# Optimization experiments

Measured on AMD Instinct MI355X. Metric: run time of the kernel, lower is better.

The kernel has to match this reference:

```python
import jax, jax.numpy as jnp
import numpy as np

NUM_USERS = 60000
NUM_ITEMS = 40000
N_NODES = NUM_USERS + NUM_ITEMS
EMBED_K = 128
E_HALF = 1_000_000  # bipartite interactions; symmetrized -> 2M directed edges


def setup_inputs() -> dict:
    key = jax.random.key(0)
    k1, k2, k3, k4, k5, k6, k7 = jax.random.split(key, 7)
    scale = 1.0 / np.sqrt(EMBED_K)  # ~ xavier_normal
    Gu = jax.random.normal(k1, (NUM_USERS, EMBED_K), jnp.float32) * scale
    Gi = jax.random.normal(k2, (NUM_ITEMS, EMBED_K), jnp.float32) * scale
    W0 = jax.random.normal(k3, (EMBED_K, EMBED_K), jnp.float32) * scale
    W1 = jax.random.normal(k4, (EMBED_K, EMBED_K), jnp.float32) * scale
    W2 = jax.random.normal(k5, (EMBED_K, EMBED_K), jnp.float32) * scale
    # bipartite user-item graph, symmetrized (items offset by NUM_USERS)
    u = jax.random.randint(k6, (E_HALF,), 0, NUM_USERS)
    it = jax.random.randint(k7, (E_HALF,), 0, NUM_ITEMS) + NUM_USERS
    src = jnp.concatenate([u, it])
    dst = jnp.concatenate([it, u])
    edge_index = jnp.stack([src, dst]).astype(jnp.int32)  # [2, 2M]
    return {"Gu": Gu, "Gi": Gi, "W0": W0, "W1": W1, "W2": W2,
            "edge_index": edge_index}


def reference(Gu, Gi, W0, W1, W2, edge_index):
    # add_self_loops=False, bias=False) -> ReLU), then split into (gu, gi).
    src, dst = edge_index[0], edge_index[1]
    n_users = Gu.shape[0]
    n_nodes = Gu.shape[0] + Gi.shape[0]
    # PyG gcn_norm (no self loops): deg = scatter(1, col); norm = d^-1/2[row]*d^-1/2[col]
    ones = jnp.ones(src.shape, Gu.dtype)
    deg = jax.ops.segment_sum(ones, dst, num_segments=n_nodes)
    dinv = jnp.where(deg > 0, jax.lax.rsqrt(jnp.maximum(deg, 1.0)), 0.0)
    norm = dinv[src] * dinv[dst]  # [E]
    x = jnp.concatenate([Gu, Gi], axis=0)  # [N, d]
    for W in (W0, W1, W2):
        h = x @ W                                   # [N, d] dense GEMM
        msg = h[src] * norm[:, None]                # [E, d] gather + scale
        x = jax.nn.relu(jax.ops.segment_sum(msg, dst, num_segments=n_nodes))
    return x[:n_users], x[n_users:]
```

## Files before the change

### kernel.cpp

```cpp
#include <hip/hip_runtime.h>
#include <hip/hip_bf16.h>

#define EMB 128
#define NPB 256
#define NB_PAD 512
#define CHUNK 4096
#define FILL_CAP 7168
#define CU_CAP 4864
#define CI_CAP 7168

typedef unsigned int uint32;
typedef unsigned long long uint64;
typedef __attribute__((ext_vector_type(8))) short bf16x8;
typedef __attribute__((ext_vector_type(4))) float f32x4;
typedef __attribute__((ext_vector_type(2))) float f32x2;
typedef __attribute__((ext_vector_type(2))) unsigned int uint32x2;

__device__ __forceinline__ ushort f2bf(float f) {
    uint32 u = __float_as_uint(f);
    return (ushort)((u + 0x7fff + ((u >> 16) & 1)) >> 16);
}
__device__ __forceinline__ uint32 pack_hi2(uint32 u0, uint32 u1) {
    return (u1 & 0xffff0000u) | (u0 >> 16);
}
__device__ __forceinline__ float blo(uint32 u) { return __uint_as_float(u << 16); }
__device__ __forceinline__ float bhi(uint32 u) { return __uint_as_float(u & 0xffff0000u); }

__device__ __forceinline__ int region_base(int b, int UB) {
    return (b < UB) ? b * CU_CAP : UB * CU_CAP + (b - UB) * CI_CAP;
}


__global__ __launch_bounds__(256) void wsplit_kernel(
    const float* __restrict__ W0, const float* __restrict__ W1,
    const float* __restrict__ W2,
    ushort* __restrict__ Whi, ushort* __restrict__ Wlo,
    int* __restrict__ gcursor, int NB, int UB) {
    int wsel = blockIdx.x >> 4, part = blockIdx.x & 15;
    if (blockIdx.x == 0) {
        for (int b = threadIdx.x; b < NB; b += 256) gcursor[b] = region_base(b, UB);
    }
    const float* W = (wsel == 0) ? W0 : (wsel == 1) ? W1 : W2;
    ushort* hiT = Whi + wsel * EMB * EMB;
    ushort* loT = Wlo + wsel * EMB * EMB;
    int i0 = part * 1024;
    #pragma unroll
    for (int j = 0; j < 4; j++) {
        int i = i0 + threadIdx.x + j * 256;
        int k = i >> 7, n = i & 127;
        float w = W[i];
        uint32 u = __float_as_uint(w);
        ushort hi = (ushort)(u >> 16);
        float hif = __uint_as_float(u & 0xffff0000u);
        ushort lo = f2bf(w - hif);
        hiT[n * EMB + k] = hi;
        loT[n * EMB + k] = lo;
    }
}


__global__ __launch_bounds__(256) void bucket_scatter_kernel(
    const int* __restrict__ src, const int* __restrict__ dst,
    int* __restrict__ gcursor, uint2* __restrict__ ebuf, int E, int NB) {
    __shared__ int cnt[NB_PAD];
    __shared__ int loff[NB_PAD];
    __shared__ int gbase[NB_PAD];
    __shared__ int pos[NB_PAD];
    __shared__ int sc[256];
    __shared__ uint2 stage[CHUNK];
    int t = threadIdx.x;
    long e0 = (long)blockIdx.x * CHUNK;
    int n = E - (int)e0; if (n > CHUNK) n = CHUNK;
    for (int b = t; b < NB_PAD; b += 256) { cnt[b] = 0; pos[b] = 0; }
    __syncthreads();
    int es[CHUNK / 256], ed[CHUNK / 256];
    #pragma unroll
    for (int i = 0; i < CHUNK / 256; i++) {
        int idx = t + i * 256;
        if (idx < n) {
            es[i] = src[e0 + idx];
            ed[i] = dst[e0 + idx];
            atomicAdd(&cnt[ed[i] >> 8], 1);
        }
    }
    __syncthreads();
    int a = cnt[2 * t], b2 = cnt[2 * t + 1];
    sc[t] = a + b2;
    __syncthreads();
    for (int off = 1; off < 256; off <<= 1) {
        int v = (t >= off) ? sc[t - off] : 0;
        __syncthreads();
        sc[t] += v;
        __syncthreads();
    }
    int excl = sc[t] - (a + b2);
    loff[2 * t] = excl;
    loff[2 * t + 1] = excl + a;
    __syncthreads();
    for (int b = t; b < NB; b += 256)
        if (cnt[b] > 0) gbase[b] = atomicAdd(&gcursor[b], cnt[b]);
    __syncthreads();
    #pragma unroll
    for (int i = 0; i < CHUNK / 256; i++) {
        int idx = t + i * 256;
        if (idx < n) {
            int b = ed[i] >> 8;
            int p = atomicAdd(&pos[b], 1);
            stage[loff[b] + p] = make_uint2((uint32)es[i], (uint32)ed[i]);
        }
    }
    __syncthreads();
    for (int i = t; i < n; i += 256) {
        uint2 e = stage[i];
        int b = (int)e.y >> 8;
        ebuf[gbase[b] + (i - loff[b])] = e;
    }
}


__global__ __launch_bounds__(256) void bucket_deg_kernel(
    const uint2* __restrict__ ebuf, const int* __restrict__ gcursor,
    uint2* __restrict__ nodeRange, float* __restrict__ dinv, int N, int UB) {
    __shared__ int cnt[NPB];
    __shared__ int sc[256];
    int t = threadIdx.x;
    int b = blockIdx.x;
    int n0 = b * NPB;
    int nn = N - n0; if (nn > NPB) nn = NPB;
    cnt[t] = 0;
    __syncthreads();
    int rb = region_base(b, UB);
    int re = gcursor[b];
    for (int e = rb + t; e < re; e += 256) {
        uint2 sd = ebuf[e];
        atomicAdd(&cnt[(int)sd.y - n0], 1);
    }
    __syncthreads();
    int c = cnt[t];
    sc[t] = c;
    __syncthreads();
    for (int off = 1; off < 256; off <<= 1) {
        int v = (t >= off) ? sc[t - off] : 0;
        __syncthreads();
        sc[t] += v;
        __syncthreads();
    }
    int excl = sc[t] - c;
    if (t < nn) {
        int s = rb + excl;
        nodeRange[n0 + t] = make_uint2((uint32)s, (uint32)(s + c));
        dinv[n0 + t] = c > 0 ? rsqrtf((float)c) : 0.0f;
    }
}


__global__ __launch_bounds__(256) void fill_ew_kernel(
    uint2* __restrict__ ebuf, const uint2* __restrict__ nodeRange,
    const int* __restrict__ gcursor, const float* __restrict__ dinv,
    int N, int UB) {
    __shared__ uint2 stage[FILL_CAP];
    __shared__ int cnt[NPB];
    __shared__ int rp[NPB];
    int t = threadIdx.x;
    int b = blockIdx.x;
    int n0 = b * NPB;
    int nn = N - n0; if (nn > NPB) nn = NPB;
    if (t < nn) { cnt[t] = 0; rp[t] = (int)nodeRange[n0 + t].x; }
    __syncthreads();
    int e0 = region_base(b, UB);
    int e1 = gcursor[b];
    int ecount = e1 - e0; if (ecount > FILL_CAP) ecount = FILL_CAP;
    for (int o = t; o < ecount; o += 256) stage[o] = ebuf[e0 + o];
    __syncthreads();
    for (int o = t; o < ecount; o += 1024) {
        uint2 sd[4]; int pos[4]; float wv[4];
        int valid = 0;
        #pragma unroll
        for (int k = 0; k < 4; k++) {
            int oo = o + k * 256;
            if (oo < ecount) { sd[k] = stage[oo]; valid = k + 1; }
        }
        #pragma unroll
        for (int k = 0; k < 4; k++)
            if (k < valid) {
                int local = (int)sd[k].y - n0;
                pos[k] = rp[local] + atomicAdd(&cnt[local], 1);
            }
        #pragma unroll
        for (int k = 0; k < 4; k++)
            if (k < valid) wv[k] = dinv[(int)sd[k].x];
        #pragma unroll
        for (int k = 0; k < 4; k++)
            if (k < valid) ebuf[pos[k]] = make_uint2(sd[k].x, __float_as_uint(wv[k]));
    }
}


template<int DI>
__device__ __forceinline__ void agg_tail2(
    const uint32x2* __restrict__ Yh2, const uint2* __restrict__ ew,
    int base, int e0, int e1, int half, int l32,
    float& a0, float& a1, float& a2, float& a3) {
    uint32 rows[DI]; float w[DI]; uint32x2 p[DI];
    #pragma unroll
    for (int k = 0; k < DI; k++) {
        int i0 = base + 2 * k, i1 = i0 + 1;
        uint2 s0 = ew[i0 < e1 ? i0 : e0];
        uint2 s1 = ew[i1 < e1 ? i1 : e0];
        rows[k] = half ? s1.x : s0.x;
        uint32 wu = half ? s1.y : s0.y;
        w[k] = (i0 + half < e1) ? __uint_as_float(wu) : 0.0f;
    }
    #pragma unroll
    for (int k = 0; k < DI; k++) p[k] = Yh2[(size_t)rows[k] * 32 + l32];
    #pragma unroll
    for (int k = 0; k < DI; k++) {
        a0 += w[k] * blo(p[k].x); a1 += w[k] * bhi(p[k].x);
        a2 += w[k] * blo(p[k].y); a3 += w[k] * bhi(p[k].y);
    }
}

__device__ __forceinline__ void agg_node2(
    const uint32x2* __restrict__ Yh2, const uint2* __restrict__ ew,
    int e0, int e1, int half, int l32,
    float& a0, float& a1, float& a2, float& a3) {
    int base = e0;
    for (; base + 16 <= e1; base += 16) {
        uint32 rows[8]; float w[8]; uint32x2 p[8];
        #pragma unroll
        for (int k = 0; k < 8; k++) {
            uint2 s0 = ew[base + 2 * k];
            uint2 s1 = ew[base + 2 * k + 1];
            rows[k] = half ? s1.x : s0.x;
            w[k] = __uint_as_float(half ? s1.y : s0.y);
        }
        #pragma unroll
        for (int k = 0; k < 8; k++) p[k] = Yh2[(size_t)rows[k] * 32 + l32];
        #pragma unroll
        for (int k = 0; k < 8; k++) {
            a0 += w[k] * blo(p[k].x); a1 += w[k] * bhi(p[k].x);
            a2 += w[k] * blo(p[k].y); a3 += w[k] * bhi(p[k].y);
        }
    }
    int rem = e1 - base;
    if (rem > 8)      agg_tail2<8>(Yh2, ew, base, e0, e1, half, l32, a0, a1, a2, a3);
    else if (rem > 4) agg_tail2<4>(Yh2, ew, base, e0, e1, half, l32, a0, a1, a2, a3);
    else if (rem > 2) agg_tail2<2>(Yh2, ew, base, e0, e1, half, l32, a0, a1, a2, a3);
    else if (rem > 0) agg_tail2<1>(Yh2, ew, base, e0, e1, half, l32, a0, a1, a2, a3);
}

__global__ __launch_bounds__(256) void agg_relu_kernel(
    const uint32x2* __restrict__ Yh2,
    const uint2* __restrict__ nodeRange, const uint2* __restrict__ ew,
    const float* __restrict__ dinv, float* __restrict__ out, int N) {
    int node = blockIdx.x * 4 + (threadIdx.x >> 6);
    if (node >= N) return;
    int lane = threadIdx.x & 63;
    int half = lane >> 5, l32 = lane & 31;
    uint2 rg = nodeRange[node];
    int e0 = __builtin_amdgcn_readfirstlane((int)rg.x);
    int e1 = __builtin_amdgcn_readfirstlane((int)rg.y);
    float a0 = 0.f, a1 = 0.f, a2 = 0.f, a3 = 0.f;
    agg_node2(Yh2, ew, e0, e1, half, l32, a0, a1, a2, a3);
    a0 += __shfl_xor(a0, 32);
    a1 += __shfl_xor(a1, 32);
    a2 += __shfl_xor(a2, 32);
    a3 += __shfl_xor(a3, 32);
    if (half == 0) {
        float wd = dinv[node];
        f32x4 r = { fmaxf(a0 * wd, 0.f), fmaxf(a1 * wd, 0.f),
                    fmaxf(a2 * wd, 0.f), fmaxf(a3 * wd, 0.f) };
        __builtin_nontemporal_store(r, (f32x4*)(out + (size_t)node * EMB + l32 * 4));
    }
}


union FragU { uint32 u[4]; bf16x8 v; };

__global__ __launch_bounds__(256, 2) void gemm_mfma_kernel(
    const float* __restrict__ A, const float* __restrict__ A2, int Msplit,
    const ushort* __restrict__ WhiT, const ushort* __restrict__ WloT,
    ushort* __restrict__ Yh, int M) {
    __shared__ float As[16][132];
    int t = threadIdx.x;
    int wv = t >> 6, lane = t & 63, quad = lane >> 4, l16 = lane & 15;

    FragU bfr[8][2];
    #pragma unroll
    for (int kc = 0; kc < 8; kc++) {
        const ushort* srcW = (kc < 4) ? WhiT : WloT;
        int kb = (kc & 3) * 32 + quad * 8;
        #pragma unroll
        for (int c = 0; c < 2; c++) {
            int n = wv * 32 + c * 16 + l16;
            const uint32* p = (const uint32*)(srcW + n * EMB + kb);
            bfr[kc][c].u[0] = p[0];
            bfr[kc][c].u[1] = p[1];
            bfr[kc][c].u[2] = p[2];
            bfr[kc][c].u[3] = p[3];
        }
    }

    int srow = t >> 4, skq = t & 15;
    int ntile = (M + 15) >> 4;
    for (int tile = blockIdx.x; tile < ntile; tile += (int)gridDim.x) {
        int r0 = tile << 4;
        __syncthreads();
        {
            float4 v0 = {0.f, 0.f, 0.f, 0.f}, v1 = v0;
            int row = r0 + srow;
            if (row < M) {
                const float* ga = (row < Msplit)
                    ? A  + (size_t)row * EMB + skq * 8
                    : A2 + (size_t)(row - Msplit) * EMB + skq * 8;
                v0 = *(const float4*)ga;
                v1 = *(const float4*)(ga + 4);
            }
            *(float4*)&As[srow][skq * 8] = v0;
            *(float4*)&As[srow][skq * 8 + 4] = v1;
        }
        __syncthreads();

        FragU ah[4], al[4];
        #pragma unroll
        for (int kc = 0; kc < 4; kc++) {
            const float* p = &As[l16][kc * 32 + quad * 8];
            float4 xa = *(const float4*)p;
            float4 xb = *(const float4*)(p + 4);
            uint32 u0 = __float_as_uint(xa.x), u1 = __float_as_uint(xa.y);
            uint32 u2 = __float_as_uint(xa.z), u3 = __float_as_uint(xa.w);
            uint32 u4 = __float_as_uint(xb.x), u5 = __float_as_uint(xb.y);
            uint32 u6 = __float_as_uint(xb.z), u7 = __float_as_uint(xb.w);
            ah[kc].u[0] = pack_hi2(u0, u1);
            ah[kc].u[1] = pack_hi2(u2, u3);
            ah[kc].u[2] = pack_hi2(u4, u5);
            ah[kc].u[3] = pack_hi2(u6, u7);
            float l0 = xa.x - __uint_as_float(u0 & 0xffff0000u);
            float l1 = xa.y - __uint_as_float(u1 & 0xffff0000u);
            float l2 = xa.z - __uint_as_float(u2 & 0xffff0000u);
            float l3 = xa.w - __uint_as_float(u3 & 0xffff0000u);
            float l4 = xb.x - __uint_as_float(u4 & 0xffff0000u);
            float l5 = xb.y - __uint_as_float(u5 & 0xffff0000u);
            float l6 = xb.z - __uint_as_float(u6 & 0xffff0000u);
            float l7 = xb.w - __uint_as_float(u7 & 0xffff0000u);
            al[kc].u[0] = pack_hi2(__float_as_uint(l0), __float_as_uint(l1));
            al[kc].u[1] = pack_hi2(__float_as_uint(l2), __float_as_uint(l3));
            al[kc].u[2] = pack_hi2(__float_as_uint(l4), __float_as_uint(l5));
            al[kc].u[3] = pack_hi2(__float_as_uint(l6), __float_as_uint(l7));
        }

        f32x4 acc0 = {0.f, 0.f, 0.f, 0.f};
        f32x4 acc1 = {0.f, 0.f, 0.f, 0.f};
        #pragma unroll
        for (int kc = 0; kc < 4; kc++) {
            acc0 = __builtin_amdgcn_mfma_f32_16x16x32_bf16(ah[kc].v, bfr[kc][0].v, acc0, 0, 0, 0);
            acc1 = __builtin_amdgcn_mfma_f32_16x16x32_bf16(ah[kc].v, bfr[kc][1].v, acc1, 0, 0, 0);
        }
        #pragma unroll
        for (int kc = 0; kc < 4; kc++) {
            acc0 = __builtin_amdgcn_mfma_f32_16x16x32_bf16(ah[kc].v, bfr[kc + 4][0].v, acc0, 0, 0, 0);
            acc1 = __builtin_amdgcn_mfma_f32_16x16x32_bf16(ah[kc].v, bfr[kc + 4][1].v, acc1, 0, 0, 0);
        }
        #pragma unroll
        for (int kc = 0; kc < 4; kc++) {
            acc0 = __builtin_amdgcn_mfma_f32_16x16x32_bf16(al[kc].v, bfr[kc][0].v, acc0, 0, 0, 0);
            acc1 = __builtin_amdgcn_mfma_f32_16x16x32_bf16(al[kc].v, bfr[kc][1].v, acc1, 0, 0, 0);
        }

        int colb = wv * 32 + l16;
        #pragma unroll
        for (int r = 0; r < 4; r++) {
            int row = r0 + quad * 4 + r;
            if (row < M) {
                Yh[(size_t)row * EMB + colb]      = f2bf(acc0[r]);
                Yh[(size_t)row * EMB + colb + 16] = f2bf(acc1[r]);
            }
        }
    }
}


extern "C" void kernel_launch(void* const* d_in, const int* in_sizes, int n_in,
                              void* d_out, int out_size, void* d_ws, size_t ws_size,
                              hipStream_t stream) {
    (void)n_in; (void)out_size; (void)ws_size;
    const float* Gu = (const float*)d_in[0];
    const float* Gi = (const float*)d_in[1];
    const float* W0 = (const float*)d_in[2];
    const float* W1 = (const float*)d_in[3];
    const float* W2 = (const float*)d_in[4];
    const int* ei = (const int*)d_in[5];

    int nu = in_sizes[0] / EMB;
    int ni = in_sizes[1] / EMB;
    int N = nu + ni;
    int E = in_sizes[5] / 2;
    const int* src = ei;
    const int* dst = ei + E;
    int NB = (N + NPB - 1) / NPB;
    int UB = nu >> 8;
    long ebufEntries = (long)UB * CU_CAP + (long)(NB - UB) * CI_CAP;

    ushort* Yh      = (ushort*)d_ws;
    uint2* ebuf     = (uint2*)(Yh + (size_t)N * EMB);
    uint2* nodeRange= ebuf + ebufEntries;
    float* dinv     = (float*)(nodeRange + N);
    int* gcursor    = (int*)(dinv + N);
    ushort* WhiT    = (ushort*)(gcursor + NB);
    ushort* WloT    = WhiT + 3 * EMB * EMB;
    float* X        = (float*)d_out;

    wsplit_kernel<<<48, 256, 0, stream>>>(W0, W1, W2, WhiT, WloT, gcursor, NB, UB);

    int ecb = (E + CHUNK - 1) / CHUNK;
    bucket_scatter_kernel<<<ecb, 256, 0, stream>>>(src, dst, gcursor, ebuf, E, NB);
    bucket_deg_kernel<<<NB, 256, 0, stream>>>(ebuf, gcursor, nodeRange, dinv, N, UB);
    fill_ew_kernel<<<NB, 256, 0, stream>>>(ebuf, nodeRange, gcursor, dinv, N, UB);

    const uint2* ew = (const uint2*)ebuf;
    int aggBlocks = (N + 3) / 4;
    const int GB = 512;

    gemm_mfma_kernel<<<GB, 256, 0, stream>>>(Gu, Gi, nu, WhiT, WloT, Yh, N);
    agg_relu_kernel<<<aggBlocks, 256, 0, stream>>>((const uint32x2*)Yh, nodeRange, ew, dinv, X, N);
    gemm_mfma_kernel<<<GB, 256, 0, stream>>>(X, X, N, WhiT + EMB * EMB, WloT + EMB * EMB, Yh, N);
    agg_relu_kernel<<<aggBlocks, 256, 0, stream>>>((const uint32x2*)Yh, nodeRange, ew, dinv, X, N);
    gemm_mfma_kernel<<<GB, 256, 0, stream>>>(X, X, N, WhiT + 2 * EMB * EMB, WloT + 2 * EMB * EMB, Yh, N);
    agg_relu_kernel<<<aggBlocks, 256, 0, stream>>>((const uint32x2*)Yh, nodeRange, ew, dinv, X, N);
}
```

Baseline: 414.4 us.

## Fold source normalization into GEMM and compact edges to 32-bit indices

```diff
diff --git a/kernel.cpp b/kernel.cpp
--- a/kernel.cpp
+++ b/kernel.cpp
@@ -10,10 +10,8 @@
 #define CI_CAP 7168
 
 typedef unsigned int uint32;
-typedef unsigned long long uint64;
 typedef __attribute__((ext_vector_type(8))) short bf16x8;
 typedef __attribute__((ext_vector_type(4))) float f32x4;
-typedef __attribute__((ext_vector_type(2))) float f32x2;
 typedef __attribute__((ext_vector_type(2))) unsigned int uint32x2;
 
 __device__ __forceinline__ ushort f2bf(float f) {
@@ -35,10 +33,11 @@
     const float* __restrict__ W0, const float* __restrict__ W1,
     const float* __restrict__ W2,
     ushort* __restrict__ Whi, ushort* __restrict__ Wlo,
-    int* __restrict__ gcursor, int NB, int UB) {
+    int* __restrict__ gcursor, uint32* __restrict__ YhZrow, int NB, int UB) {
     int wsel = blockIdx.x >> 4, part = blockIdx.x & 15;
     if (blockIdx.x == 0) {
         for (int b = threadIdx.x; b < NB; b += 256) gcursor[b] = region_base(b, UB);
+        if (threadIdx.x < 64) YhZrow[threadIdx.x] = 0;
     }
     const float* W = (wsel == 0) ? W0 : (wsel == 1) ? W1 : W2;
     ushort* hiT = Whi + wsel * EMB * EMB;
@@ -61,7 +60,7 @@
 
 __global__ __launch_bounds__(256) void bucket_scatter_kernel(
     const int* __restrict__ src, const int* __restrict__ dst,
-    int* __restrict__ gcursor, uint2* __restrict__ ebuf, int E, int NB) {
+    int* __restrict__ gcursor, uint32* __restrict__ ebuf, int E, int NB) {
     __shared__ int cnt[NB_PAD];
     __shared__ int loff[NB_PAD];
     __shared__ int gbase[NB_PAD];
@@ -113,146 +112,123 @@
     for (int i = t; i < n; i += 256) {
         uint2 e = stage[i];
         int b = (int)e.y >> 8;
-        ebuf[gbase[b] + (i - loff[b])] = e;
-    }
-}
-
-
-__global__ __launch_bounds__(256) void bucket_deg_kernel(
-    const uint2* __restrict__ ebuf, const int* __restrict__ gcursor,
+        ebuf[gbase[b] + (i - loff[b])] = ((e.y & 255u) << 24) | e.x;
+    }
+}
+
+
+__global__ __launch_bounds__(256) void build_kernel(
+    uint32* __restrict__ ebuf, const int* __restrict__ gcursor,
     uint2* __restrict__ nodeRange, float* __restrict__ dinv, int N, int UB) {
+    __shared__ uint32 stage[FILL_CAP];
     __shared__ int cnt[NPB];
     __shared__ int sc[256];
-    int t = threadIdx.x;
-    int b = blockIdx.x;
-    int n0 = b * NPB;
-    int nn = N - n0; if (nn > NPB) nn = NPB;
-    cnt[t] = 0;
-    __syncthreads();
-    int rb = region_base(b, UB);
-    int re = gcursor[b];
-    for (int e = rb + t; e < re; e += 256) {
-        uint2 sd = ebuf[e];
-        atomicAdd(&cnt[(int)sd.y - n0], 1);
-    }
-    __syncthreads();
-    int c = cnt[t];
-    sc[t] = c;
-    __syncthreads();
-    for (int off = 1; off < 256; off <<= 1) {
-        int v = (t >= off) ? sc[t - off] : 0;
-        __syncthreads();
-        sc[t] += v;
-        __syncthreads();
-    }
-    int excl = sc[t] - c;
-    if (t < nn) {
-        int s = rb + excl;
-        nodeRange[n0 + t] = make_uint2((uint32)s, (uint32)(s + c));
-        dinv[n0 + t] = c > 0 ? rsqrtf((float)c) : 0.0f;
-    }
-}
-
-
-__global__ __launch_bounds__(256) void fill_ew_kernel(
-    uint2* __restrict__ ebuf, const uint2* __restrict__ nodeRange,
-    const int* __restrict__ gcursor, const float* __restrict__ dinv,
-    int N, int UB) {
-    __shared__ uint2 stage[FILL_CAP];
-    __shared__ int cnt[NPB];
     __shared__ int rp[NPB];
     int t = threadIdx.x;
     int b = blockIdx.x;
     int n0 = b * NPB;
     int nn = N - n0; if (nn > NPB) nn = NPB;
-    if (t < nn) { cnt[t] = 0; rp[t] = (int)nodeRange[n0 + t].x; }
-    __syncthreads();
-    int e0 = region_base(b, UB);
-    int e1 = gcursor[b];
-    int ecount = e1 - e0; if (ecount > FILL_CAP) ecount = FILL_CAP;
-    for (int o = t; o < ecount; o += 256) stage[o] = ebuf[e0 + o];
+    int rb = region_base(b, UB);
+    int re = gcursor[b];
+    int ecount = re - rb; if (ecount > FILL_CAP) ecount = FILL_CAP;
+    for (int o = t; o < ecount; o += 256) stage[o] = ebuf[rb + o];
+    cnt[t] = 0;
+    __syncthreads();
+    for (int o = t; o < ecount; o += 256) atomicAdd(&cnt[stage[o] >> 24], 1);
+    __syncthreads();
+    int c = cnt[t];
+    sc[t] = c;
+    __syncthreads();
+    for (int off = 1; off < 256; off <<= 1) {
+        int v = (t >= off) ? sc[t - off] : 0;
+        __syncthreads();
+        sc[t] += v;
+        __syncthreads();
+    }
+    int excl = sc[t] - c;
+    int start = rb + excl;
+    if (t < nn) {
+        nodeRange[n0 + t] = make_uint2((uint32)start, (uint32)(start + c));
+        dinv[n0 + t] = c > 0 ? rsqrtf((float)c) : 0.0f;
+    }
+    rp[t] = start;
+    cnt[t] = 0;
     __syncthreads();
     for (int o = t; o < ecount; o += 1024) {
-        uint2 sd[4]; int pos[4]; float wv[4];
+        uint32 v[4]; int pos[4];
         int valid = 0;
         #pragma unroll
         for (int k = 0; k < 4; k++) {
             int oo = o + k * 256;
-            if (oo < ecount) { sd[k] = stage[oo]; valid = k + 1; }
+            if (oo < ecount) { v[k] = stage[oo]; valid = k + 1; }
         }
         #pragma unroll
         for (int k = 0; k < 4; k++)
-            if (k < valid) {
-                int local = (int)sd[k].y - n0;
-                pos[k] = rp[local] + atomicAdd(&cnt[local], 1);
-            }
+            if (k < valid) pos[k] = rp[v[k] >> 24] + atomicAdd(&cnt[v[k] >> 24], 1);
         #pragma unroll
         for (int k = 0; k < 4; k++)
-            if (k < valid) wv[k] = dinv[(int)sd[k].x];
-        #pragma unroll
-        for (int k = 0; k < 4; k++)
-            if (k < valid) ebuf[pos[k]] = make_uint2(sd[k].x, __float_as_uint(wv[k]));
+            if (k < valid) ebuf[pos[k]] = v[k] & 0x00FFFFFFu;
     }
 }
 
 
 template<int DI>
 __device__ __forceinline__ void agg_tail2(
-    const uint32x2* __restrict__ Yh2, const uint2* __restrict__ ew,
-    int base, int e0, int e1, int half, int l32,
+    const uint32x2* __restrict__ Yh2, const uint32* __restrict__ ew,
+    int base, int e0, int e1, int half, int l32, int ZR,
     float& a0, float& a1, float& a2, float& a3) {
-    uint32 rows[DI]; float w[DI]; uint32x2 p[DI];
+    uint32 rows[DI]; uint32x2 p[DI];
     #pragma unroll
     for (int k = 0; k < DI; k++) {
         int i0 = base + 2 * k, i1 = i0 + 1;
-        uint2 s0 = ew[i0 < e1 ? i0 : e0];
-        uint2 s1 = ew[i1 < e1 ? i1 : e0];
-        rows[k] = half ? s1.x : s0.x;
-        uint32 wu = half ? s1.y : s0.y;
-        w[k] = (i0 + half < e1) ? __uint_as_float(wu) : 0.0f;
+        uint32 r0 = ew[i0 < e1 ? i0 : e0];
+        uint32 r1 = ew[i1 < e1 ? i1 : e0];
+        uint32 sel = half ? r1 : r0;
+        rows[k] = (i0 + half < e1) ? sel : (uint32)ZR;
     }
     #pragma unroll
     for (int k = 0; k < DI; k++) p[k] = Yh2[(size_t)rows[k] * 32 + l32];
     #pragma unroll
     for (int k = 0; k < DI; k++) {
-        a0 += w[k] * blo(p[k].x); a1 += w[k] * bhi(p[k].x);
-        a2 += w[k] * blo(p[k].y); a3 += w[k] * bhi(p[k].y);
+        a0 += blo(p[k].x); a1 += bhi(p[k].x);
+        a2 += blo(p[k].y); a3 += bhi(p[k].y);
     }
 }
 
 __device__ __forceinline__ void agg_node2(
-    const uint32x2* __restrict__ Yh2, const uint2* __restrict__ ew,
-    int e0, int e1, int half, int l32,
+    const uint32x2* __restrict__ Yh2, const uint32* __restrict__ ew,
+    int e0, int e1, int half, int l32, int ZR,
     float& a0, float& a1, float& a2, float& a3) {
     int base = e0;
     for (; base + 16 <= e1; base += 16) {
-        uint32 rows[8]; float w[8]; uint32x2 p[8];
+        uint32 rows[8]; uint32x2 p[8];
         #pragma unroll
         for (int k = 0; k < 8; k++) {
-            uint2 s0 = ew[base + 2 * k];
-            uint2 s1 = ew[base + 2 * k + 1];
-            rows[k] = half ? s1.x : s0.x;
-            w[k] = __uint_as_float(half ? s1.y : s0.y);
+            uint32 r0 = ew[base + 2 * k];
+            uint32 r1 = ew[base + 2 * k + 1];
+            rows[k] = half ? r1 : r0;
         }
         #pragma unroll
         for (int k = 0; k < 8; k++) p[k] = Yh2[(size_t)rows[k] * 32 + l32];
         #pragma unroll
         for (int k = 0; k < 8; k++) {
-            a0 += w[k] * blo(p[k].x); a1 += w[k] * bhi(p[k].x);
-            a2 += w[k] * blo(p[k].y); a3 += w[k] * bhi(p[k].y);
+            a0 += blo(p[k].x); a1 += bhi(p[k].x);
+            a2 += blo(p[k].y); a3 += bhi(p[k].y);
         }
     }
     int rem = e1 - base;
-    if (rem > 8)      agg_tail2<8>(Yh2, ew, base, e0, e1, half, l32, a0, a1, a2, a3);
-    else if (rem > 4) agg_tail2<4>(Yh2, ew, base, e0, e1, half, l32, a0, a1, a2, a3);
-    else if (rem > 2) agg_tail2<2>(Yh2, ew, base, e0, e1, half, l32, a0, a1, a2, a3);
-    else if (rem > 0) agg_tail2<1>(Yh2, ew, base, e0, e1, half, l32, a0, a1, a2, a3);
-}
-
-__global__ __launch_bounds__(256) void agg_relu_kernel(
+    if (rem > 8)      agg_tail2<8>(Yh2, ew, base, e0, e1, half, l32, ZR, a0, a1, a2, a3);
+    else if (rem > 4) agg_tail2<4>(Yh2, ew, base, e0, e1, half, l32, ZR, a0, a1, a2, a3);
+    else if (rem > 2) agg_tail2<2>(Yh2, ew, base, e0, e1, half, l32, ZR, a0, a1, a2, a3);
+    else if (rem > 0) agg_tail2<1>(Yh2, ew, base, e0, e1, half, l32, ZR, a0, a1, a2, a3);
+}
+
+template<bool FINAL>
+__global__ __launch_bounds__(256) void agg_kernel(
     const uint32x2* __restrict__ Yh2,
-    const uint2* __restrict__ nodeRange, const uint2* __restrict__ ew,
-    const float* __restrict__ dinv, float* __restrict__ out, int N) {
+    const uint2* __restrict__ nodeRange, const uint32* __restrict__ ew,
+    const float* __restrict__ dinv, float* __restrict__ out,
+    uint32* __restrict__ Xhi, uint32* __restrict__ Xlo, int N) {
     int node = blockIdx.x * 4 + (threadIdx.x >> 6);
     if (node >= N) return;
     int lane = threadIdx.x & 63;
@@ -261,26 +237,40 @@
     int e0 = __builtin_amdgcn_readfirstlane((int)rg.x);
     int e1 = __builtin_amdgcn_readfirstlane((int)rg.y);
     float a0 = 0.f, a1 = 0.f, a2 = 0.f, a3 = 0.f;
-    agg_node2(Yh2, ew, e0, e1, half, l32, a0, a1, a2, a3);
+    agg_node2(Yh2, ew, e0, e1, half, l32, N, a0, a1, a2, a3);
     a0 += __shfl_xor(a0, 32);
     a1 += __shfl_xor(a1, 32);
     a2 += __shfl_xor(a2, 32);
     a3 += __shfl_xor(a3, 32);
     if (half == 0) {
         float wd = dinv[node];
-        f32x4 r = { fmaxf(a0 * wd, 0.f), fmaxf(a1 * wd, 0.f),
-                    fmaxf(a2 * wd, 0.f), fmaxf(a3 * wd, 0.f) };
-        __builtin_nontemporal_store(r, (f32x4*)(out + (size_t)node * EMB + l32 * 4));
+        float v0 = fmaxf(a0 * wd, 0.f), v1 = fmaxf(a1 * wd, 0.f);
+        float v2 = fmaxf(a2 * wd, 0.f), v3 = fmaxf(a3 * wd, 0.f);
+        if (FINAL) {
+            f32x4 r = { v0, v1, v2, v3 };
+            __builtin_nontemporal_store(r, (f32x4*)(out + (size_t)node * EMB + l32 * 4));
+        } else {
+            uint32 u0 = __float_as_uint(v0), u1 = __float_as_uint(v1);
+            uint32 u2 = __float_as_uint(v2), u3 = __float_as_uint(v3);
+            uint32x2 hw = { pack_hi2(u0, u1), pack_hi2(u2, u3) };
+            uint32 lo0 = f2bf(v0 - __uint_as_float(u0 & 0xffff0000u));
+            uint32 lo1 = f2bf(v1 - __uint_as_float(u1 & 0xffff0000u));
+            uint32 lo2 = f2bf(v2 - __uint_as_float(u2 & 0xffff0000u));
+            uint32 lo3 = f2bf(v3 - __uint_as_float(u3 & 0xffff0000u));
+            uint32x2 lw = { lo0 | (lo1 << 16), lo2 | (lo3 << 16) };
+            *(uint32x2*)(Xhi + (size_t)node * 64 + l32 * 2) = hw;
+            *(uint32x2*)(Xlo + (size_t)node * 64 + l32 * 2) = lw;
+        }
     }
 }
 
 
 union FragU { uint32 u[4]; bf16x8 v; };
 
-__global__ __launch_bounds__(256, 2) void gemm_mfma_kernel(
+__global__ __launch_bounds__(256, 2) void gemm_split_kernel(
     const float* __restrict__ A, const float* __restrict__ A2, int Msplit,
     const ushort* __restrict__ WhiT, const ushort* __restrict__ WloT,
-    ushort* __restrict__ Yh, int M) {
+    const float* __restrict__ dinv, ushort* __restrict__ Yh, int M) {
     __shared__ float As[16][132];
     int t = threadIdx.x;
     int wv = t >> 6, lane = t & 63, quad = lane >> 4, l16 = lane & 15;
@@ -367,13 +357,85 @@
             acc1 = __builtin_amdgcn_mfma_f32_16x16x32_bf16(al[kc].v, bfr[kc][1].v, acc1, 0, 0, 0);
         }
 
+        float4 dv = *(const float4*)(dinv + r0 + quad * 4);
         int colb = wv * 32 + l16;
         #pragma unroll
         for (int r = 0; r < 4; r++) {
             int row = r0 + quad * 4 + r;
             if (row < M) {
-                Yh[(size_t)row * EMB + colb]      = f2bf(acc0[r]);
-                Yh[(size_t)row * EMB + colb + 16] = f2bf(acc1[r]);
+                float d = (&dv.x)[r];
+                Yh[(size_t)row * EMB + colb]      = f2bf(acc0[r] * d);
+                Yh[(size_t)row * EMB + colb + 16] = f2bf(acc1[r] * d);
+            }
+        }
+    }
+}
+
+__global__ __launch_bounds__(256, 2) void gemm_pre_kernel(
+    const uint32* __restrict__ Ahi, const uint32* __restrict__ Alo,
+    const ushort* __restrict__ WhiT, const ushort* __restrict__ WloT,
+    const float* __restrict__ dinv, ushort* __restrict__ Yh, int M) {
+    __shared__ ushort Ah[16][136];
+    __shared__ ushort Al[16][136];
+    int t = threadIdx.x;
+    int wv = t >> 6, lane = t & 63, quad = lane >> 4, l16 = lane & 15;
+
+    FragU bfr[8][2];
+    #pragma unroll
+    for (int kc = 0; kc < 8; kc++) {
+        const ushort* srcW = (kc < 4) ? WhiT : WloT;
+        int kb = (kc & 3) * 32 + quad * 8;
+        #pragma unroll
+        for (int c = 0; c < 2; c++) {
+            int n = wv * 32 + c * 16 + l16;
+            const uint32* p = (const uint32*)(srcW + n * EMB + kb);
+            bfr[kc][c].u[0] = p[0];
+            bfr[kc][c].u[1] = p[1];
+            bfr[kc][c].u[2] = p[2];
+            bfr[kc][c].u[3] = p[3];
+        }
+    }
+
+    int srow = t >> 4, skq = t & 15;
+    int ntile = (M + 15) >> 4;
+    for (int tile = blockIdx.x; tile < ntile; tile += (int)gridDim.x) {
+        int r0 = tile << 4;
+        __syncthreads();
+        {
+            uint4 vh = {0, 0, 0, 0}, vl = vh;
+            int row = r0 + srow;
+            if (row < M) {
+                vh = *(const uint4*)(Ahi + (size_t)row * 64 + skq * 4);
+                vl = *(const uint4*)(Alo + (size_t)row * 64 + skq * 4);
+            }
+            *(uint4*)&Ah[srow][skq * 8] = vh;
+            *(uint4*)&Al[srow][skq * 8] = vl;
+        }
+        __syncthreads();
+
+        f32x4 acc0 = {0.f, 0.f, 0.f, 0.f};
+        f32x4 acc1 = {0.f, 0.f, 0.f, 0.f};
+        #pragma unroll
+        for (int kc = 0; kc < 4; kc++) {
+            bf16x8 ah = *(const bf16x8*)&Ah[l16][kc * 32 + quad * 8];
+            bf16x8 al = *(const bf16x8*)&Al[l16][kc * 32 + quad * 8];
+            acc0 = __builtin_amdgcn_mfma_f32_16x16x32_bf16(ah, bfr[kc][0].v, acc0, 0, 0, 0);
+            acc1 = __builtin_amdgcn_mfma_f32_16x16x32_bf16(ah, bfr[kc][1].v, acc1, 0, 0, 0);
+            acc0 = __builtin_amdgcn_mfma_f32_16x16x32_bf16(ah, bfr[kc + 4][0].v, acc0, 0, 0, 0);
+            acc1 = __builtin_amdgcn_mfma_f32_16x16x32_bf16(ah, bfr[kc + 4][1].v, acc1, 0, 0, 0);
+            acc0 = __builtin_amdgcn_mfma_f32_16x16x32_bf16(al, bfr[kc][0].v, acc0, 0, 0, 0);
+            acc1 = __builtin_amdgcn_mfma_f32_16x16x32_bf16(al, bfr[kc][1].v, acc1, 0, 0, 0);
+        }
+
+        float4 dv = *(const float4*)(dinv + r0 + quad * 4);
+        int colb = wv * 32 + l16;
+        #pragma unroll
+        for (int r = 0; r < 4; r++) {
+            int row = r0 + quad * 4 + r;
+            if (row < M) {
+                float d = (&dv.x)[r];
+                Yh[(size_t)row * EMB + colb]      = f2bf(acc0[r] * d);
+                Yh[(size_t)row * EMB + colb + 16] = f2bf(acc1[r] * d);
             }
         }
     }
@@ -402,29 +464,36 @@
     long ebufEntries = (long)UB * CU_CAP + (long)(NB - UB) * CI_CAP;
 
     ushort* Yh      = (ushort*)d_ws;
-    uint2* ebuf     = (uint2*)(Yh + (size_t)N * EMB);
-    uint2* nodeRange= ebuf + ebufEntries;
+    uint32* ebuf    = (uint32*)(Yh + (size_t)(N + 1) * EMB);
+    uint2* nodeRange= (uint2*)(ebuf + ebufEntries);
     float* dinv     = (float*)(nodeRange + N);
     int* gcursor    = (int*)(dinv + N);
     ushort* WhiT    = (ushort*)(gcursor + NB);
     ushort* WloT    = WhiT + 3 * EMB * EMB;
+    uint32* Xhi     = (uint32*)d_out;
+    uint32* Xlo     = Xhi + (size_t)N * 64;
     float* X        = (float*)d_out;
 
-    wsplit_kernel<<<48, 256, 0, stream>>>(W0, W1, W2, WhiT, WloT, gcursor, NB, UB);
+    wsplit_kernel<<<48, 256, 0, stream>>>(W0, W1, W2, WhiT, WloT, gcursor,
+                                          (uint32*)(Yh + (size_t)N * EMB), NB, UB);
 
     int ecb = (E + CHUNK - 1) / CHUNK;
     bucket_scatter_kernel<<<ecb, 256, 0, stream>>>(src, dst, gcursor, ebuf, E, NB);
-    bucket_deg_kernel<<<NB, 256, 0, stream>>>(ebuf, gcursor, nodeRange, dinv, N, UB);
-    fill_ew_kernel<<<NB, 256, 0, stream>>>(ebuf, nodeRange, gcursor, dinv, N, UB);
-
-    const uint2* ew = (const uint2*)ebuf;
+    build_kernel<<<NB, 256, 0, stream>>>(ebuf, gcursor, nodeRange, dinv, N, UB);
+
+    const uint32* ew = (const uint32*)ebuf;
     int aggBlocks = (N + 3) / 4;
     const int GB = 512;
 
-    gemm_mfma_kernel<<<GB, 256, 0, stream>>>(Gu, Gi, nu, WhiT, WloT, Yh, N);
-    agg_relu_kernel<<<aggBlocks, 256, 0, stream>>>((const uint32x2*)Yh, nodeRange, ew, dinv, X, N);
-    gemm_mfma_kernel<<<GB, 256, 0, stream>>>(X, X, N, WhiT + EMB * EMB, WloT + EMB * EMB, Yh, N);
-    agg_relu_kernel<<<aggBlocks, 256, 0, stream>>>((const uint32x2*)Yh, nodeRange, ew, dinv, X, N);
-    gemm_mfma_kernel<<<GB, 256, 0, stream>>>(X, X, N, WhiT + 2 * EMB * EMB, WloT + 2 * EMB * EMB, Yh, N);
-    agg_relu_kernel<<<aggBlocks, 256, 0, stream>>>((const uint32x2*)Yh, nodeRange, ew, dinv, X, N);
-}
+    gemm_split_kernel<<<GB, 256, 0, stream>>>(Gu, Gi, nu, WhiT, WloT, dinv, Yh, N);
+    agg_kernel<false><<<aggBlocks, 256, 0, stream>>>((const uint32x2*)Yh, nodeRange, ew,
+                                                     dinv, nullptr, Xhi, Xlo, N);
+    gemm_pre_kernel<<<GB, 256, 0, stream>>>(Xhi, Xlo, WhiT + EMB * EMB, WloT + EMB * EMB,
+                                            dinv, Yh, N);
+    agg_kernel<false><<<aggBlocks, 256, 0, stream>>>((const uint32x2*)Yh, nodeRange, ew,
+                                                     dinv, nullptr, Xhi, Xlo, N);
+    gemm_pre_kernel<<<GB, 256, 0, stream>>>(Xhi, Xlo, WhiT + 2 * EMB * EMB, WloT + 2 * EMB * EMB,
+                                            dinv, Yh, N);
+    agg_kernel<true><<<aggBlocks, 256, 0, stream>>>((const uint32x2*)Yh, nodeRange, ew,
+                                                    dinv, X, nullptr, nullptr, N);
+}
```

Measured after the change: 401.3 us. -3.2%, faster.
